# Optimization experiments

Hardware: AMD Instinct MI355X
Metric: run time of the kernel (lower is better)

The kernel has to match this reference:

```python
import jax, jax.numpy as jnp
import numpy as np

B, L, N, C = 4, 12, 1024, 3
D = 32          # num_hidden
ND = 32         # node_hidden
TE = 10         # time_emb_dim
ST = 96         # tsformer/st hidden feat
GH = 64         # estimation-gate hidden
KS = 2          # diffusion orders (k_s)
NUM_FEAT = 1
TID, DIW = 288, 7


def random_walk(adj):
    # adj: [B,N,N]; (D^-1)(A+I) row-normalized random-walk matrix
    n = adj.shape[-1]
    adj = adj + jnp.eye(n, dtype=adj.dtype)[None]
    d = adj.sum(axis=2)
    d_inv = jnp.where(d == 0, 0.0, 1.0 / d)
    return adj * d_inv[:, :, None]  # diag_embed(d_inv) @ adj == row scaling


def setup_inputs() -> dict:
    key = jax.random.key(0)
    ks = jax.random.split(key, 16)
    s = 0.05
    return {
        "history_data": jax.random.uniform(ks[0], (B, L, N, C), dtype=jnp.float32),
        "hidden_states_st": jax.random.normal(ks[1], (B, N, L, ST), dtype=jnp.float32),
        "sampled_adj": jax.random.uniform(ks[2], (B, N, N), dtype=jnp.float32),
        "W_emb": jax.random.normal(ks[3], (NUM_FEAT, D), dtype=jnp.float32) * s,
        "b_emb": jnp.zeros((D,), jnp.float32),
        "W_st": jax.random.normal(ks[4], (ST, D), dtype=jnp.float32) * s,
        "b_st": jnp.zeros((D,), jnp.float32),
        "TiD_emb": jax.random.normal(ks[5], (TID, TE), dtype=jnp.float32) * s,
        "DiW_emb": jax.random.normal(ks[6], (DIW, TE), dtype=jnp.float32) * s,
        "node_emb_u": jax.random.normal(ks[7], (N, ND), dtype=jnp.float32) * s,
        "node_emb_d": jax.random.normal(ks[8], (N, ND), dtype=jnp.float32) * s,
        "W_g1": jax.random.normal(ks[9], (2 * TE + 2 * ND, GH), dtype=jnp.float32) * s,
        "b_g1": jnp.zeros((GH,), jnp.float32),
        "W_g2": jax.random.normal(ks[10], (GH, 1), dtype=jnp.float32) * s,
        "b_g2": jnp.zeros((1,), jnp.float32),
        "W_dif": jax.random.normal(ks[11], ((1 + 3 * KS) * D, D), dtype=jnp.float32) * s,
        "b_dif": jnp.zeros((D,), jnp.float32),
    }


def reference(history_data, hidden_states_st, sampled_adj, W_emb, b_emb, W_st, b_st,
              TiD_emb, DiW_emb, node_emb_u, node_emb_d, W_g1, b_g1, W_g2, b_g2,
              W_dif, b_dif):
    # --- prepare inputs: time/node embedding gathers (D2STGNN._prepare_inputs) ---
    X = history_data.at[..., 2].multiply(1.0 / 7.0)
    t_idx = (X[..., NUM_FEAT] * TID).astype(jnp.int32)       # [B,L,N]
    d_idx = (X[..., NUM_FEAT + 1] * DIW).astype(jnp.int32)   # [B,L,N]
    T_D = TiD_emb[t_idx]   # [B,L,N,TE]
    D_W = DiW_emb[d_idx]   # [B,L,N,TE]
    Xf = X[..., :NUM_FEAT]  # [B,L,N,1]

    # --- graph construction (static self-adaptive + random-walk normalized learn graphs) ---
    static = jax.nn.softmax(jax.nn.relu(node_emb_d @ node_emb_u.T), axis=1)  # [N,N]
    rw_fwd = random_walk(sampled_adj)                       # [B,N,N]
    rw_bwd = random_walk(jnp.swapaxes(sampled_adj, -1, -2)) # [B,N,N]

    # --- input embedding + st hidden fusion ---
    H = jnp.einsum('blnf,fd->blnd', Xf, W_emb) + b_emb
    H_st = jnp.einsum('bnlk,kd->bnld', hidden_states_st, W_st) + b_st
    H = jax.nn.relu(H + jnp.transpose(H_st, (0, 2, 1, 3)))  # [B,L,N,D]

    # --- estimation (spatial) gate: sigmoid(FC(relu(FC([T_D,D_W,E_u,E_d])))) * X ---
    eu = jnp.broadcast_to(node_emb_u[None, None], (B, L, N, ND))
    ed = jnp.broadcast_to(node_emb_d[None, None], (B, L, N, ND))
    gate_feat = jnp.concatenate([T_D, D_W, eu, ed], axis=-1)  # [B,L,N,2TE+2ND]
    gate = jax.nn.sigmoid(jax.nn.relu(gate_feat @ W_g1 + b_g1) @ W_g2 + b_g2)  # [B,L,N,1]
    X_spa = H * gate

    # --- diffusion graph convolution over supports, KS orders each ---
    supports = [jnp.broadcast_to(static[None], (B, N, N)), rw_fwd, rw_bwd]
    outs = [X_spa]
    for A in supports:
        Z = X_spa
        for _ in range(KS):
            Z = jnp.einsum('bnm,blmd->blnd', A, Z)
            outs.append(Z)
    Hcat = jnp.concatenate(outs, axis=-1)  # [B,L,N,(1+3*KS)*D]
    out = Hcat @ W_dif + b_dif             # [B,L,N,D]
    return out
```

## Files before the change

kernel.cpp:

```cpp
#include <hip/hip_runtime.h>
#include <hip/hip_bf16.h>
#include <cstdint>

#define NN 1024
#define BBATCH 4
#define LLEN 12
#define NJ 384
#define TIDC 288
#define DIWC 7

typedef __attribute__((ext_vector_type(8))) short short8;
typedef __attribute__((ext_vector_type(4))) float f32x4;

__device__ inline ushort f2bf(float f) {
    unsigned u = __float_as_uint(f);
    u += 0x7FFFu + ((u >> 16) & 1u);
    return (ushort)(u >> 16);
}
__device__ inline float bf2f(ushort u) { return __uint_as_float(((unsigned)u) << 16); }

__global__ __launch_bounds__(256) void k_static(const float* __restrict__ emb_u,
                                                const float* __restrict__ emb_d,
                                                ushort* __restrict__ S_bf) {
    int i = blockIdx.x;
    int t = threadIdx.x;
    __shared__ float drow[32];
    __shared__ float red[256];
    if (t < 32) drow[t] = emb_d[i * 32 + t];
    __syncthreads();
    float v[4];
    float lsum = 0.f;
    for (int jj = 0; jj < 4; ++jj) {
        int j = jj * 256 + t;
        const float4* u4 = reinterpret_cast<const float4*>(emb_u + (size_t)j * 32);
        float acc = 0.f;
#pragma unroll
        for (int k4 = 0; k4 < 8; ++k4) {
            float4 u = u4[k4];
            acc += drow[k4 * 4 + 0] * u.x + drow[k4 * 4 + 1] * u.y +
                   drow[k4 * 4 + 2] * u.z + drow[k4 * 4 + 3] * u.w;
        }
        acc = fmaxf(acc, 0.f);
        v[jj] = __expf(acc);
        lsum += v[jj];
    }
    red[t] = lsum;
    __syncthreads();
    for (int s = 128; s > 0; s >>= 1) {
        if (t < s) red[t] += red[t + s];
        __syncthreads();
    }
    float inv = 1.f / red[0];
    for (int jj = 0; jj < 4; ++jj) S_bf[(size_t)i * NN + jj * 256 + t] = f2bf(v[jj] * inv);
}

__global__ __launch_bounds__(256) void k_adj_pre(const float* __restrict__ adj,
                                                 ushort* __restrict__ adjF,
                                                 ushort* __restrict__ adjT,
                                                 float* __restrict__ rs,
                                                 float* __restrict__ cs) {
    __shared__ float tile[64][65];
    int b = blockIdx.z;
    int r0 = blockIdx.y * 64, c0 = blockIdx.x * 64;
    int t = threadIdx.x;
    int col = (t & 15) * 4, rb = t >> 4;
#pragma unroll
    for (int i = 0; i < 4; ++i) {
        int r = rb + i * 16;
        float4 v = *reinterpret_cast<const float4*>(&adj[((size_t)b * NN + r0 + r) * NN + c0 + col]);
        tile[r][col] = v.x; tile[r][col + 1] = v.y; tile[r][col + 2] = v.z; tile[r][col + 3] = v.w;
        unsigned lo = (unsigned)f2bf(v.x) | ((unsigned)f2bf(v.y) << 16);
        unsigned hi = (unsigned)f2bf(v.z) | ((unsigned)f2bf(v.w) << 16);
        *reinterpret_cast<uint2*>(&adjF[((size_t)b * NN + r0 + r) * NN + c0 + col]) = make_uint2(lo, hi);
    }
    __syncthreads();
    {
        int r4 = t >> 2, q4 = t & 3;
        float s1 = 0.f;
#pragma unroll
        for (int c = 0; c < 16; ++c) s1 += tile[r4][q4 * 16 + c];
        s1 += __shfl_xor(s1, 1, 64);
        s1 += __shfl_xor(s1, 2, 64);
        if (q4 == 0) atomicAdd(&rs[b * NN + r0 + r4], s1);
        float s2 = 0.f;
#pragma unroll
        for (int rr = 0; rr < 16; ++rr) s2 += tile[q4 * 16 + rr][r4];
        s2 += __shfl_xor(s2, 1, 64);
        s2 += __shfl_xor(s2, 2, 64);
        if (q4 == 0) atomicAdd(&cs[b * NN + c0 + r4], s2);
    }
    int j = t >> 2, ch = t & 3;
    short8 o0, o1;
#pragma unroll
    for (int q = 0; q < 8; ++q) o0[q] = (short)f2bf(tile[ch * 16 + q][j]);
#pragma unroll
    for (int q = 0; q < 8; ++q) o1[q] = (short)f2bf(tile[ch * 16 + 8 + q][j]);
    size_t orow = ((size_t)b * NN + c0 + j) * NN + r0 + ch * 16;
    *(short8*)&adjT[orow] = o0;
    *(short8*)&adjT[orow + 8] = o1;
}

__global__ __launch_bounds__(64) void k_gate_pre(const float* __restrict__ emb_u,
                                                 const float* __restrict__ emb_d,
                                                 const float* __restrict__ W_g1,
                                                 const float* __restrict__ b_g1,
                                                 const float* __restrict__ TiD,
                                                 const float* __restrict__ DiW,
                                                 const float* __restrict__ W_st,
                                                 const float* __restrict__ W_dif,
                                                 float* __restrict__ U1, float* __restrict__ T1,
                                                 float* __restrict__ D1,
                                                 ushort* __restrict__ WstT_bf,
                                                 ushort* __restrict__ WdT_bf) {
    int r = blockIdx.x;
    int h = threadIdx.x;
    if (r < NN) {
        float acc = b_g1[h];
        for (int i = 0; i < 32; ++i) acc = fmaf(emb_u[r * 32 + i], W_g1[(20 + i) * 64 + h], acc);
        for (int i = 0; i < 32; ++i) acc = fmaf(emb_d[r * 32 + i], W_g1[(52 + i) * 64 + h], acc);
        U1[r * 64 + h] = acc;
    } else if (r < NN + TIDC) {
        int tt = r - NN;
        float acc = 0.f;
        for (int i = 0; i < 10; ++i) acc = fmaf(TiD[tt * 10 + i], W_g1[i * 64 + h], acc);
        T1[tt * 64 + h] = acc;
    } else if (r < NN + TIDC + DIWC) {
        int dd = r - (NN + TIDC);
        float acc = 0.f;
        for (int i = 0; i < 10; ++i) acc = fmaf(DiW[dd * 10 + i], W_g1[(10 + i) * 64 + h], acc);
        D1[dd * 64 + h] = acc;
    } else if (r == NN + TIDC + DIWC) {
        for (int i = h; i < 32 * 96; i += 64) WstT_bf[i] = f2bf(W_st[(i % 96) * 32 + i / 96]);
    } else {
        for (int i = h; i < 32 * 224; i += 64) WdT_bf[i] = f2bf(W_dif[(i % 224) * 32 + i / 224]);
    }
}

__global__ __launch_bounds__(256) void k_xspa(const float* __restrict__ hist,
                                              const float* __restrict__ hs,
                                              const float* __restrict__ W_emb,
                                              const float* __restrict__ b_emb,
                                              const float* __restrict__ b_st,
                                              const float* __restrict__ U1,
                                              const float* __restrict__ T1,
                                              const float* __restrict__ D1,
                                              const float* __restrict__ W_g2,
                                              const float* __restrict__ b_g2,
                                              const float* __restrict__ b_dif,
                                              const ushort* __restrict__ WstT_bf,
                                              const ushort* __restrict__ WdT_bf,
                                              ushort* __restrict__ XT,
                                              float* __restrict__ out) {
    __shared__ __align__(16) ushort hsm[64][104];
    __shared__ __align__(16) ushort Wst_s[32][104];
    __shared__ __align__(16) ushort Hs_bf[64][40];
    __shared__ __align__(16) ushort W0_s[32][40];
    __shared__ float gateL[64];
    __shared__ float histL[192];
    int t = threadIdx.x;
    int n0 = blockIdx.x * 64;
    int l = blockIdx.y;
    int b = blockIdx.z;
    for (int i = t; i < 384; i += 256) {
        int d = i / 12, c = i % 12;
        *(short8*)&Wst_s[d][c * 8] = *(const short8*)&WstT_bf[d * 96 + c * 8];
    }
    if (t < 128) {
        int d = t >> 2, c = t & 3;
        *(short8*)&W0_s[d][c * 8] = *(const short8*)&WdT_bf[d * 224 + c * 8];
    }
    if (t < 48)
        *(float4*)&histL[t * 4] =
            *(const float4*)&hist[(((size_t)b * LLEN + l) * NN + n0) * 3 + t * 4];
#pragma unroll
    for (int rr = 0; rr < 6; ++rr) {
        int i = t + 256 * rr;
        int s = i / 24, c = i % 24;
        float4 v = *(const float4*)&hs[(((size_t)b * NN + n0 + s) * LLEN + l) * 96 + c * 4];
        ushort4 u;
        u.x = f2bf(v.x); u.y = f2bf(v.y); u.z = f2bf(v.z); u.w = f2bf(v.w);
        *(ushort4*)&hsm[s][c * 4] = u;
    }
    __syncthreads();
    {
        int s = t >> 2, q = t & 3;
        int n = n0 + s;
        float x1 = histL[s * 3 + 1];
        float x2 = histL[s * 3 + 2] * (1.f / 7.f);
        int ti = (int)(x1 * 288.f); ti = ti < 0 ? 0 : (ti > 287 ? 287 : ti);
        int di = (int)(x2 * 7.f);   di = di < 0 ? 0 : (di > 6 ? 6 : di);
        const float* up = U1 + n * 64 + q * 16;
        const float* tp = T1 + ti * 64 + q * 16;
        const float* dp = D1 + di * 64 + q * 16;
        const float* wp = W_g2 + q * 16;
        float a = 0.f;
#pragma unroll
        for (int hh = 0; hh < 16; ++hh)
            a = fmaf(fmaxf(up[hh] + tp[hh] + dp[hh], 0.f), wp[hh], a);
        a += __shfl_xor(a, 1, 64);
        a += __shfl_xor(a, 2, 64);
        if (q == 0) gateL[s] = 1.f / (1.f + __expf(-(a + b_g2[0])));
    }
    int w = t >> 6, l6 = t & 63, lr = l6 & 15, lg = l6 >> 4;
    f32x4 hacc[2];
    hacc[0] = (f32x4){0.f, 0.f, 0.f, 0.f};
    hacc[1] = (f32x4){0.f, 0.f, 0.f, 0.f};
#pragma unroll
    for (int kc = 0; kc < 3; ++kc) {
        short8 a = *(const short8*)&hsm[w * 16 + lr][kc * 32 + lg * 8];
        short8 b0 = *(const short8*)&Wst_s[lr][kc * 32 + lg * 8];
        short8 b1 = *(const short8*)&Wst_s[16 + lr][kc * 32 + lg * 8];
        hacc[0] = __builtin_amdgcn_mfma_f32_16x16x32_bf16(a, b0, hacc[0], 0, 0, 0);
        hacc[1] = __builtin_amdgcn_mfma_f32_16x16x32_bf16(a, b1, hacc[1], 0, 0, 0);
    }
#pragma unroll
    for (int h = 0; h < 2; ++h) {
        int d = h * 16 + lr;
        float we = W_emb[d];
        float bb = b_emb[d] + b_st[d];
#pragma unroll
        for (int r = 0; r < 4; ++r) {
            int s = w * 16 + lg * 4 + r;
            float v = fmaxf(fmaf(histL[s * 3], we, bb) + hacc[h][r], 0.f);
            Hs_bf[s][d] = f2bf(v);
        }
    }
    __syncthreads();
    f32x4 oacc[2];
    oacc[0] = (f32x4){0.f, 0.f, 0.f, 0.f};
    oacc[1] = (f32x4){0.f, 0.f, 0.f, 0.f};
    {
        short8 a = *(const short8*)&Hs_bf[w * 16 + lr][lg * 8];
        short8 b0 = *(const short8*)&W0_s[lr][lg * 8];
        short8 b1 = *(const short8*)&W0_s[16 + lr][lg * 8];
        oacc[0] = __builtin_amdgcn_mfma_f32_16x16x32_bf16(a, b0, oacc[0], 0, 0, 0);
        oacc[1] = __builtin_amdgcn_mfma_f32_16x16x32_bf16(a, b1, oacc[1], 0, 0, 0);
    }
#pragma unroll
    for (int h = 0; h < 2; ++h) {
        int d = h * 16 + lr;
        float bd = b_dif[d];
#pragma unroll
        for (int r = 0; r < 4; ++r) {
            int s = w * 16 + lg * 4 + r;
            out[(((size_t)b * LLEN + l) * NN + n0 + s) * 32 + d] = fmaf(gateL[s], oacc[h][r], bd);
        }
    }
    {
        int dd = t >> 3, c = t & 7;
        short8 v;
#pragma unroll
        for (int i = 0; i < 8; ++i) {
            int s = c * 8 + i;
            v[i] = (short)f2bf(bf2f(Hs_bf[s][dd]) * gateL[s]);
        }
        *(short8*)&XT[((size_t)b * NJ + l * 32 + dd) * NN + n0 + c * 8] = v;
    }
}

#define DIFF_LOAD(ra, rw, kt)                                          \
    {                                                                  \
        const ushort* qA = pA + (size_t)(kt) * 64;                     \
        const ushort* qW = pW + (size_t)(kt) * 64;                     \
        _Pragma("unroll") for (int i = 0; i < 4; ++i)                  \
            ra[i] = *(const short8*)(qA + i * 8);                      \
        _Pragma("unroll") for (int i = 0; i < 2; ++i)                  \
            rw[i] = *(const short8*)(qW + i * 8);                      \
    }
#define DIFF_WRITE(buf, ra, rw)                                        \
    {                                                                  \
        _Pragma("unroll") for (int i = 0; i < 4; ++i)                  \
            *(short8*)&As[buf][arow * 64 + (((ac + i) ^ (arow & 7)) * 8)] = ra[i]; \
        _Pragma("unroll") for (int i = 0; i < 2; ++i)                  \
            *(short8*)&Ws[buf][wrow * 64 + (((wc + i) ^ (wrow & 7)) * 8)] = rw[i]; \
    }
#define DIFF_COMPUTE(buf)                                              \
    {                                                                  \
        _Pragma("unroll") for (int kk = 0; kk < 2; ++kk) {             \
            short8 af[4], bff[2];                                      \
            _Pragma("unroll") for (int mf = 0; mf < 4; ++mf) {         \
                int row = wm * 64 + mf * 16 + lr;                      \
                af[mf] = *(const short8*)&As[buf][row * 64 + (((kk * 4 + lg) ^ (row & 7)) * 8)]; \
            }                                                          \
            _Pragma("unroll") for (int nf = 0; nf < 2; ++nf) {         \
                int row = wn * 32 + nf * 16 + lr;                      \
                bff[nf] = *(const short8*)&Ws[buf][row * 64 + (((kk * 4 + lg) ^ (row & 7)) * 8)]; \
            }                                                          \
            _Pragma("unroll") for (int mf = 0; mf < 4; ++mf) {         \
                acc[mf][0] = __builtin_amdgcn_mfma_f32_16x16x32_bf16(af[mf], bff[0], acc[mf][0], 0, 0, 0); \
                acc[mf][1] = __builtin_amdgcn_mfma_f32_16x16x32_bf16(af[mf], bff[1], acc[mf][1], 0, 0, 0); \
            }                                                          \
        }                                                              \
    }

__global__ __launch_bounds__(256) void k_diff3(const ushort* __restrict__ S_bf,
                                               const ushort* __restrict__ adjF,
                                               const ushort* __restrict__ adjT,
                                               const float* __restrict__ rs,
                                               const float* __restrict__ cs,
                                               const ushort* __restrict__ In0,
                                               int in_per_chain,
                                               ushort* __restrict__ Out0) {
    __shared__ __align__(16) ushort As[2][128 * 64];
    __shared__ __align__(16) ushort Ws[2][64 * 64];
    int bid = blockIdx.x + 3 * blockIdx.y + 48 * blockIdx.z;
    int swz = (bid & 7) * 72 + (bid >> 3);
    int zz = swz / 48;
    int rem = swz % 48;
    int xx = rem >> 4, yy = rem & 15;
    int s = zz >> 2, b = zz & 3;
    int j0 = xx * 128;
    int n0 = yy * 64;
    const size_t ZT = (size_t)BBATCH * NJ * NN;
    const ushort* Wb = (s == 0) ? S_bf
                     : (s == 1) ? adjF + (size_t)b * NN * NN
                                : adjT + (size_t)b * NN * NN;
    const float* deg = (s == 0) ? nullptr : (s == 1 ? rs : cs);
    const ushort* Inb = In0 + (in_per_chain ? (size_t)s * ZT : 0) + (size_t)b * NJ * NN;
    ushort* Outb = Out0 + (size_t)s * ZT + (size_t)b * NJ * NN;

    int t = threadIdx.x;
    int arow = t >> 1, ac = (t & 1) * 4;
    int wrow = t >> 2, wc = (t & 3) * 2;
    const ushort* pA = Inb + (size_t)(j0 + arow) * NN + ac * 8;
    const ushort* pW = Wb + (size_t)(n0 + wrow) * NN + wc * 8;
    int w = t >> 6, wm = w >> 1, wn = w & 1;
    int l = t & 63, lr = l & 15, lg = l >> 4;
    f32x4 acc[4][2];
#pragma unroll
    for (int i = 0; i < 4; ++i)
#pragma unroll
        for (int j = 0; j < 2; ++j) acc[i][j] = (f32x4){0.f, 0.f, 0.f, 0.f};

    short8 raA[4], rwA[2], raB[4], rwB[2];
    DIFF_LOAD(raA, rwA, 0);
    DIFF_LOAD(raB, rwB, 1);
    DIFF_WRITE(0, raA, rwA);
    __syncthreads();
    int cur = 0;
#pragma unroll 1
    for (int kt2 = 0; kt2 < 16; kt2 += 2) {
        if (kt2 + 2 < 16) DIFF_LOAD(raA, rwA, kt2 + 2);
        DIFF_COMPUTE(cur);
        DIFF_WRITE(cur ^ 1, raB, rwB);
        __syncthreads();
        cur ^= 1;
        if (kt2 + 3 < 16) DIFF_LOAD(raB, rwB, kt2 + 3);
        DIFF_COMPUTE(cur);
        if (kt2 + 2 < 16) DIFF_WRITE(cur ^ 1, raA, rwA);
        __syncthreads();
        cur ^= 1;
    }
    bool resid = (deg != nullptr);
#pragma unroll
    for (int nf = 0; nf < 2; ++nf) {
        int n_g = n0 + wn * 32 + nf * 16 + lr;
        float scale = 1.f;
        if (resid) scale = 1.f / (deg[b * NN + n_g] + 1.f);
#pragma unroll
        for (int mf = 0; mf < 4; ++mf) {
#pragma unroll
            for (int r = 0; r < 4; ++r) {
                int j_g = j0 + wm * 64 + mf * 16 + lg * 4 + r;
                float v = acc[mf][nf][r];
                if (resid) v += bf2f(Inb[(size_t)j_g * NN + n_g]);
                v *= scale;
                Outb[(size_t)j_g * NN + n_g] = f2bf(v);
            }
        }
    }
}

__global__ __launch_bounds__(256) void k_zmfma(const ushort* __restrict__ Z1,
                                               const ushort* __restrict__ Z2,
                                               const ushort* __restrict__ WdT_bf,
                                               float* __restrict__ out) {
    __shared__ __align__(16) ushort zT[64][200];
    __shared__ __align__(16) ushort Wd_s[32][200];
    const size_t ZT = (size_t)BBATCH * NJ * NN;
    int t = threadIdx.x;
    int n0 = blockIdx.x * 64;
    int l = blockIdx.y;
    int b = blockIdx.z;
    for (int i = t; i < 768; i += 256) {
        int d = i / 24, c = i % 24;
        *(short8*)&Wd_s[d][c * 8] = *(const short8*)&WdT_bf[d * 224 + 32 + c * 8];
    }
    {
        int j = t >> 3, ch = t & 7;
#pragma unroll
        for (int c = 0; c < 6; ++c) {
            const ushort* Zp = ((c & 1) ? Z2 : Z1) + (size_t)(c >> 1) * ZT;
            short8 v = *(const short8*)&Zp[((size_t)b * NJ + l * 32 + j) * NN + n0 + ch * 8];
#pragma unroll
            for (int q = 0; q < 8; ++q) zT[ch * 8 + q][c * 32 + j] = (ushort)v[q];
        }
    }
    __syncthreads();
    int w = t >> 6, l6 = t & 63, lr = l6 & 15, lg = l6 >> 4;
    f32x4 acc[2];
    acc[0] = (f32x4){0.f, 0.f, 0.f, 0.f};
    acc[1] = (f32x4){0.f, 0.f, 0.f, 0.f};
#pragma unroll
    for (int kc = 0; kc < 6; ++kc) {
        short8 a = *(const short8*)&zT[w * 16 + lr][kc * 32 + lg * 8];
        short8 b0 = *(const short8*)&Wd_s[lr][kc * 32 + lg * 8];
        short8 b1 = *(const short8*)&Wd_s[16 + lr][kc * 32 + lg * 8];
        acc[0] = __builtin_amdgcn_mfma_f32_16x16x32_bf16(a, b0, acc[0], 0, 0, 0);
        acc[1] = __builtin_amdgcn_mfma_f32_16x16x32_bf16(a, b1, acc[1], 0, 0, 0);
    }
#pragma unroll
    for (int h = 0; h < 2; ++h) {
        int d = h * 16 + lr;
#pragma unroll
        for (int r = 0; r < 4; ++r) {
            int s = w * 16 + lg * 4 + r;
            size_t oi = (((size_t)b * LLEN + l) * NN + n0 + s) * 32 + d;
            out[oi] += acc[h][r];
        }
    }
}

extern "C" void kernel_launch(void* const* d_in, const int* in_sizes, int n_in,
                              void* d_out, int out_size, void* d_ws, size_t ws_size,
                              hipStream_t stream) {
    (void)in_sizes; (void)n_in; (void)out_size; (void)ws_size;
    const float* hist  = (const float*)d_in[0];
    const float* hs    = (const float*)d_in[1];
    const float* adj   = (const float*)d_in[2];
    const float* W_emb = (const float*)d_in[3];
    const float* b_emb = (const float*)d_in[4];
    const float* W_st  = (const float*)d_in[5];
    const float* b_st  = (const float*)d_in[6];
    const float* TiD   = (const float*)d_in[7];
    const float* DiW   = (const float*)d_in[8];
    const float* emb_u = (const float*)d_in[9];
    const float* emb_d = (const float*)d_in[10];
    const float* W_g1  = (const float*)d_in[11];
    const float* b_g1  = (const float*)d_in[12];
    const float* W_g2  = (const float*)d_in[13];
    const float* b_g2  = (const float*)d_in[14];
    const float* W_dif = (const float*)d_in[15];
    const float* b_dif = (const float*)d_in[16];
    float* out = (float*)d_out;

    uint8_t* w8 = (uint8_t*)d_ws;
    ushort* adjF = (ushort*)w8;
    ushort* adjT = (ushort*)(w8 + 8388608);
    ushort* S_bf = (ushort*)(w8 + 16777216);
    ushort* XT   = (ushort*)(w8 + 18874368);
    ushort* Z1   = (ushort*)(w8 + 22020096);
    ushort* Z2   = (ushort*)(w8 + 31457280);
    float*  rs   = (float*)(w8 + 40894464);
    float*  cs   = (float*)(w8 + 40910848);
    float*  U1   = (float*)(w8 + 40927232);
    float*  T1   = (float*)(w8 + 41189376);
    float*  D1   = (float*)(w8 + 41263104);
    ushort* WstT_bf = (ushort*)(w8 + 41264896);
    ushort* WdT_bf  = (ushort*)(w8 + 41271040);

    hipMemsetAsync(rs, 0, 2 * BBATCH * NN * sizeof(float), stream);
    k_adj_pre<<<dim3(16, 16, 4), 256, 0, stream>>>(adj, adjF, adjT, rs, cs);
    k_gate_pre<<<NN + TIDC + DIWC + 2, 64, 0, stream>>>(emb_u, emb_d, W_g1, b_g1, TiD, DiW,
                                                        W_st, W_dif, U1, T1, D1, WstT_bf, WdT_bf);
    k_static<<<NN, 256, 0, stream>>>(emb_u, emb_d, S_bf);
    k_xspa<<<dim3(16, 12, 4), 256, 0, stream>>>(hist, hs, W_emb, b_emb, b_st, U1, T1, D1,
                                                W_g2, b_g2, b_dif, WstT_bf, WdT_bf, XT, out);
    dim3 dgrid(3, 16, 12);
    k_diff3<<<dgrid, 256, 0, stream>>>(S_bf, adjF, adjT, rs, cs, XT, 0, Z1);
    k_diff3<<<dgrid, 256, 0, stream>>>(S_bf, adjF, adjT, rs, cs, Z1, 1, Z2);
    k_zmfma<<<dim3(16, 12, 4), 256, 0, stream>>>(Z1, Z2, WdT_bf, out);
}
```

Measured before the change: 211.5 us.

## Merge preprocessing kernels and stage diffusion tiles via direct global-to-LDS loads

Merges the three preprocessing kernels (adjacency transpose and degree sums, static softmax adjacency, gate precompute) into one launch that branches on block index. This cuts launch overhead and lets the independent pieces run at the same time. The diffusion GEMM replaces its register-staged double buffer with global_load_lds async copies straight into swizzled LDS. That removes the register round trip and simplifies the loop to one stage per k-tile. The risk is that the async LDS loads need correct waitcnt and barrier ordering, and the per-lane swizzle layout must match what the compute path reads.

```diff
diff --git a/kernel.cpp b/kernel.cpp
--- a/kernel.cpp
+++ b/kernel.cpp
@@ -12,6 +12,9 @@
 typedef __attribute__((ext_vector_type(8))) short short8;
 typedef __attribute__((ext_vector_type(4))) float f32x4;
 
+typedef __attribute__((address_space(1))) const void* gas_ptr;
+typedef __attribute__((address_space(3))) void* las_ptr;
+
 __device__ inline ushort f2bf(float f) {
     unsigned u = __float_as_uint(f);
     u += 0x7FFFu + ((u >> 16) & 1u);
@@ -19,120 +22,120 @@
 }
 __device__ inline float bf2f(ushort u) { return __uint_as_float(((unsigned)u) << 16); }
 
-__global__ __launch_bounds__(256) void k_static(const float* __restrict__ emb_u,
-                                                const float* __restrict__ emb_d,
-                                                ushort* __restrict__ S_bf) {
-    int i = blockIdx.x;
+__global__ __launch_bounds__(256) void k_pre(const float* __restrict__ adj,
+                                             ushort* __restrict__ adjF,
+                                             ushort* __restrict__ adjT,
+                                             float* __restrict__ rs,
+                                             float* __restrict__ cs,
+                                             const float* __restrict__ emb_u,
+                                             const float* __restrict__ emb_d,
+                                             ushort* __restrict__ S_bf,
+                                             const float* __restrict__ W_g1,
+                                             const float* __restrict__ b_g1,
+                                             const float* __restrict__ TiD,
+                                             const float* __restrict__ DiW,
+                                             const float* __restrict__ W_st,
+                                             const float* __restrict__ W_dif,
+                                             float* __restrict__ U1,
+                                             float* __restrict__ T1,
+                                             float* __restrict__ D1,
+                                             ushort* __restrict__ WstT_bf,
+                                             ushort* __restrict__ WdT_bf) {
+    __shared__ float smem[64 * 65];
+    int bid = blockIdx.x;
     int t = threadIdx.x;
-    __shared__ float drow[32];
-    __shared__ float red[256];
-    if (t < 32) drow[t] = emb_d[i * 32 + t];
-    __syncthreads();
-    float v[4];
-    float lsum = 0.f;
-    for (int jj = 0; jj < 4; ++jj) {
-        int j = jj * 256 + t;
-        const float4* u4 = reinterpret_cast<const float4*>(emb_u + (size_t)j * 32);
-        float acc = 0.f;
-#pragma unroll
-        for (int k4 = 0; k4 < 8; ++k4) {
-            float4 u = u4[k4];
-            acc += drow[k4 * 4 + 0] * u.x + drow[k4 * 4 + 1] * u.y +
-                   drow[k4 * 4 + 2] * u.z + drow[k4 * 4 + 3] * u.w;
-        }
-        acc = fmaxf(acc, 0.f);
-        v[jj] = __expf(acc);
-        lsum += v[jj];
-    }
-    red[t] = lsum;
-    __syncthreads();
-    for (int s = 128; s > 0; s >>= 1) {
-        if (t < s) red[t] += red[t + s];
+    if (bid < 1024) {
+        float (*tile)[65] = (float(*)[65])smem;
+        int b = bid >> 8;
+        int r0 = ((bid >> 4) & 15) * 64, c0 = (bid & 15) * 64;
+        int col = (t & 15) * 4, rb = t >> 4;
+#pragma unroll
+        for (int i = 0; i < 4; ++i) {
+            int r = rb + i * 16;
+            float4 v = *reinterpret_cast<const float4*>(&adj[((size_t)b * NN + r0 + r) * NN + c0 + col]);
+            tile[r][col] = v.x; tile[r][col + 1] = v.y; tile[r][col + 2] = v.z; tile[r][col + 3] = v.w;
+            unsigned lo = (unsigned)f2bf(v.x) | ((unsigned)f2bf(v.y) << 16);
+            unsigned hi = (unsigned)f2bf(v.z) | ((unsigned)f2bf(v.w) << 16);
+            *reinterpret_cast<uint2*>(&adjF[((size_t)b * NN + r0 + r) * NN + c0 + col]) = make_uint2(lo, hi);
+        }
         __syncthreads();
-    }
-    float inv = 1.f / red[0];
-    for (int jj = 0; jj < 4; ++jj) S_bf[(size_t)i * NN + jj * 256 + t] = f2bf(v[jj] * inv);
-}
-
-__global__ __launch_bounds__(256) void k_adj_pre(const float* __restrict__ adj,
-                                                 ushort* __restrict__ adjF,
-                                                 ushort* __restrict__ adjT,
-                                                 float* __restrict__ rs,
-                                                 float* __restrict__ cs) {
-    __shared__ float tile[64][65];
-    int b = blockIdx.z;
-    int r0 = blockIdx.y * 64, c0 = blockIdx.x * 64;
-    int t = threadIdx.x;
-    int col = (t & 15) * 4, rb = t >> 4;
-#pragma unroll
-    for (int i = 0; i < 4; ++i) {
-        int r = rb + i * 16;
-        float4 v = *reinterpret_cast<const float4*>(&adj[((size_t)b * NN + r0 + r) * NN + c0 + col]);
-        tile[r][col] = v.x; tile[r][col + 1] = v.y; tile[r][col + 2] = v.z; tile[r][col + 3] = v.w;
-        unsigned lo = (unsigned)f2bf(v.x) | ((unsigned)f2bf(v.y) << 16);
-        unsigned hi = (unsigned)f2bf(v.z) | ((unsigned)f2bf(v.w) << 16);
-        *reinterpret_cast<uint2*>(&adjF[((size_t)b * NN + r0 + r) * NN + c0 + col]) = make_uint2(lo, hi);
-    }
-    __syncthreads();
-    {
-        int r4 = t >> 2, q4 = t & 3;
-        float s1 = 0.f;
-#pragma unroll
-        for (int c = 0; c < 16; ++c) s1 += tile[r4][q4 * 16 + c];
-        s1 += __shfl_xor(s1, 1, 64);
-        s1 += __shfl_xor(s1, 2, 64);
-        if (q4 == 0) atomicAdd(&rs[b * NN + r0 + r4], s1);
-        float s2 = 0.f;
-#pragma unroll
-        for (int rr = 0; rr < 16; ++rr) s2 += tile[q4 * 16 + rr][r4];
-        s2 += __shfl_xor(s2, 1, 64);
-        s2 += __shfl_xor(s2, 2, 64);
-        if (q4 == 0) atomicAdd(&cs[b * NN + c0 + r4], s2);
-    }
-    int j = t >> 2, ch = t & 3;
-    short8 o0, o1;
-#pragma unroll
-    for (int q = 0; q < 8; ++q) o0[q] = (short)f2bf(tile[ch * 16 + q][j]);
-#pragma unroll
-    for (int q = 0; q < 8; ++q) o1[q] = (short)f2bf(tile[ch * 16 + 8 + q][j]);
-    size_t orow = ((size_t)b * NN + c0 + j) * NN + r0 + ch * 16;
-    *(short8*)&adjT[orow] = o0;
-    *(short8*)&adjT[orow + 8] = o1;
-}
-
-__global__ __launch_bounds__(64) void k_gate_pre(const float* __restrict__ emb_u,
-                                                 const float* __restrict__ emb_d,
-                                                 const float* __restrict__ W_g1,
-                                                 const float* __restrict__ b_g1,
-                                                 const float* __restrict__ TiD,
-                                                 const float* __restrict__ DiW,
-                                                 const float* __restrict__ W_st,
-                                                 const float* __restrict__ W_dif,
-                                                 float* __restrict__ U1, float* __restrict__ T1,
-                                                 float* __restrict__ D1,
-                                                 ushort* __restrict__ WstT_bf,
-                                                 ushort* __restrict__ WdT_bf) {
-    int r = blockIdx.x;
-    int h = threadIdx.x;
-    if (r < NN) {
-        float acc = b_g1[h];
-        for (int i = 0; i < 32; ++i) acc = fmaf(emb_u[r * 32 + i], W_g1[(20 + i) * 64 + h], acc);
-        for (int i = 0; i < 32; ++i) acc = fmaf(emb_d[r * 32 + i], W_g1[(52 + i) * 64 + h], acc);
-        U1[r * 64 + h] = acc;
-    } else if (r < NN + TIDC) {
-        int tt = r - NN;
-        float acc = 0.f;
-        for (int i = 0; i < 10; ++i) acc = fmaf(TiD[tt * 10 + i], W_g1[i * 64 + h], acc);
-        T1[tt * 64 + h] = acc;
-    } else if (r < NN + TIDC + DIWC) {
-        int dd = r - (NN + TIDC);
-        float acc = 0.f;
-        for (int i = 0; i < 10; ++i) acc = fmaf(DiW[dd * 10 + i], W_g1[(10 + i) * 64 + h], acc);
-        D1[dd * 64 + h] = acc;
-    } else if (r == NN + TIDC + DIWC) {
-        for (int i = h; i < 32 * 96; i += 64) WstT_bf[i] = f2bf(W_st[(i % 96) * 32 + i / 96]);
+        {
+            int r4 = t >> 2, q4 = t & 3;
+            float s1 = 0.f;
+#pragma unroll
+            for (int c = 0; c < 16; ++c) s1 += tile[r4][q4 * 16 + c];
+            s1 += __shfl_xor(s1, 1, 64);
+            s1 += __shfl_xor(s1, 2, 64);
+            if (q4 == 0) atomicAdd(&rs[b * NN + r0 + r4], s1);
+            float s2 = 0.f;
+#pragma unroll
+            for (int rr = 0; rr < 16; ++rr) s2 += tile[q4 * 16 + rr][r4];
+            s2 += __shfl_xor(s2, 1, 64);
+            s2 += __shfl_xor(s2, 2, 64);
+            if (q4 == 0) atomicAdd(&cs[b * NN + c0 + r4], s2);
+        }
+        int j = t >> 2, ch = t & 3;
+        short8 o0, o1;
+#pragma unroll
+        for (int q = 0; q < 8; ++q) o0[q] = (short)f2bf(tile[ch * 16 + q][j]);
+#pragma unroll
+        for (int q = 0; q < 8; ++q) o1[q] = (short)f2bf(tile[ch * 16 + 8 + q][j]);
+        size_t orow = ((size_t)b * NN + c0 + j) * NN + r0 + ch * 16;
+        *(short8*)&adjT[orow] = o0;
+        *(short8*)&adjT[orow + 8] = o1;
+    } else if (bid < 2048) {
+        int i = bid - 1024;
+        float* drow = smem;
+        float* red = smem + 32;
+        if (t < 32) drow[t] = emb_d[i * 32 + t];
+        __syncthreads();
+        float v[4];
+        float lsum = 0.f;
+        for (int jj = 0; jj < 4; ++jj) {
+            int j = jj * 256 + t;
+            const float4* u4 = reinterpret_cast<const float4*>(emb_u + (size_t)j * 32);
+            float acc = 0.f;
+#pragma unroll
+            for (int k4 = 0; k4 < 8; ++k4) {
+                float4 u = u4[k4];
+                acc += drow[k4 * 4 + 0] * u.x + drow[k4 * 4 + 1] * u.y +
+                       drow[k4 * 4 + 2] * u.z + drow[k4 * 4 + 3] * u.w;
+            }
+            acc = fmaxf(acc, 0.f);
+            v[jj] = __expf(acc);
+            lsum += v[jj];
+        }
+        red[t] = lsum;
+        __syncthreads();
+        for (int s = 128; s > 0; s >>= 1) {
+            if (t < s) red[t] += red[t + s];
+            __syncthreads();
+        }
+        float inv = 1.f / red[0];
+        for (int jj = 0; jj < 4; ++jj) S_bf[(size_t)i * NN + jj * 256 + t] = f2bf(v[jj] * inv);
     } else {
-        for (int i = h; i < 32 * 224; i += 64) WdT_bf[i] = f2bf(W_dif[(i % 224) * 32 + i / 224]);
+        int r = (bid - 2048) * 4 + (t >> 6);
+        int h = t & 63;
+        if (r < NN) {
+            float acc = b_g1[h];
+            for (int i = 0; i < 32; ++i) acc = fmaf(emb_u[r * 32 + i], W_g1[(20 + i) * 64 + h], acc);
+            for (int i = 0; i < 32; ++i) acc = fmaf(emb_d[r * 32 + i], W_g1[(52 + i) * 64 + h], acc);
+            U1[r * 64 + h] = acc;
+        } else if (r < NN + TIDC) {
+            int tt = r - NN;
+            float acc = 0.f;
+            for (int i = 0; i < 10; ++i) acc = fmaf(TiD[tt * 10 + i], W_g1[i * 64 + h], acc);
+            T1[tt * 64 + h] = acc;
+        } else if (r < NN + TIDC + DIWC) {
+            int dd = r - (NN + TIDC);
+            float acc = 0.f;
+            for (int i = 0; i < 10; ++i) acc = fmaf(DiW[dd * 10 + i], W_g1[(10 + i) * 64 + h], acc);
+            D1[dd * 64 + h] = acc;
+        } else if (r == NN + TIDC + DIWC) {
+            for (int i = h; i < 32 * 96; i += 64) WstT_bf[i] = f2bf(W_st[(i % 96) * 32 + i / 96]);
+        } else if (r == NN + TIDC + DIWC + 1) {
+            for (int i = h; i < 32 * 224; i += 64) WdT_bf[i] = f2bf(W_dif[(i % 224) * 32 + i / 224]);
+        }
     }
 }
 
@@ -258,21 +261,18 @@
     }
 }
 
-#define DIFF_LOAD(ra, rw, kt)                                          \
-    {                                                                  \
-        const ushort* qA = pA + (size_t)(kt) * 64;                     \
-        const ushort* qW = pW + (size_t)(kt) * 64;                     \
-        _Pragma("unroll") for (int i = 0; i < 4; ++i)                  \
-            ra[i] = *(const short8*)(qA + i * 8);                      \
-        _Pragma("unroll") for (int i = 0; i < 2; ++i)                  \
-            rw[i] = *(const short8*)(qW + i * 8);                      \
-    }
-#define DIFF_WRITE(buf, ra, rw)                                        \
-    {                                                                  \
-        _Pragma("unroll") for (int i = 0; i < 4; ++i)                  \
-            *(short8*)&As[buf][arow * 64 + (((ac + i) ^ (arow & 7)) * 8)] = ra[i]; \
-        _Pragma("unroll") for (int i = 0; i < 2; ++i)                  \
-            *(short8*)&Ws[buf][wrow * 64 + (((wc + i) ^ (wrow & 7)) * 8)] = rw[i]; \
+#define STAGE(buf, kt)                                                              \
+    {                                                                               \
+        const ushort* gA = pA + (size_t)(kt) * 64;                                  \
+        const ushort* gW = pW + (size_t)(kt) * 64;                                  \
+        _Pragma("unroll") for (int i = 0; i < 4; ++i)                               \
+            __builtin_amdgcn_global_load_lds(                                        \
+                (gas_ptr)(gA + aoff[i]),                                             \
+                (las_ptr)&As[buf][(w * 32 + i * 8) * 64], 16, 0, 0);                \
+        _Pragma("unroll") for (int i = 0; i < 2; ++i)                               \
+            __builtin_amdgcn_global_load_lds(                                        \
+                (gas_ptr)(gW + woff[i]),                                             \
+                (las_ptr)&Ws[buf][(w * 16 + i * 8) * 64], 16, 0, 0);                \
     }
 #define DIFF_COMPUTE(buf)                                              \
     {                                                                  \
@@ -320,34 +320,35 @@
     ushort* Outb = Out0 + (size_t)s * ZT + (size_t)b * NJ * NN;
 
     int t = threadIdx.x;
-    int arow = t >> 1, ac = (t & 1) * 4;
-    int wrow = t >> 2, wc = (t & 3) * 2;
-    const ushort* pA = Inb + (size_t)(j0 + arow) * NN + ac * 8;
-    const ushort* pW = Wb + (size_t)(n0 + wrow) * NN + wc * 8;
     int w = t >> 6, wm = w >> 1, wn = w & 1;
     int l = t & 63, lr = l & 15, lg = l >> 4;
+    int rl = l >> 3, c8 = l & 7;
+    size_t aoff[4], woff[2];
+#pragma unroll
+    for (int i = 0; i < 4; ++i) {
+        int row = w * 32 + i * 8 + rl;
+        aoff[i] = (size_t)row * NN + (size_t)((c8 ^ (row & 7)) * 8);
+    }
+#pragma unroll
+    for (int i = 0; i < 2; ++i) {
+        int row = w * 16 + i * 8 + rl;
+        woff[i] = (size_t)row * NN + (size_t)((c8 ^ (row & 7)) * 8);
+    }
+    const ushort* pA = Inb + (size_t)j0 * NN;
+    const ushort* pW = Wb + (size_t)n0 * NN;
     f32x4 acc[4][2];
 #pragma unroll
     for (int i = 0; i < 4; ++i)
 #pragma unroll
         for (int j = 0; j < 2; ++j) acc[i][j] = (f32x4){0.f, 0.f, 0.f, 0.f};
 
-    short8 raA[4], rwA[2], raB[4], rwB[2];
-    DIFF_LOAD(raA, rwA, 0);
-    DIFF_LOAD(raB, rwB, 1);
-    DIFF_WRITE(0, raA, rwA);
+    STAGE(0, 0);
     __syncthreads();
     int cur = 0;
 #pragma unroll 1
-    for (int kt2 = 0; kt2 < 16; kt2 += 2) {
-        if (kt2 + 2 < 16) DIFF_LOAD(raA, rwA, kt2 + 2);
+    for (int kt = 0; kt < 16; ++kt) {
+        if (kt < 15) STAGE(cur ^ 1, kt + 1);
         DIFF_COMPUTE(cur);
-        DIFF_WRITE(cur ^ 1, raB, rwB);
-        __syncthreads();
-        cur ^= 1;
-        if (kt2 + 3 < 16) DIFF_LOAD(raB, rwB, kt2 + 3);
-        DIFF_COMPUTE(cur);
-        if (kt2 + 2 < 16) DIFF_WRITE(cur ^ 1, raA, rwA);
         __syncthreads();
         cur ^= 1;
     }
@@ -460,10 +461,9 @@
     ushort* WdT_bf  = (ushort*)(w8 + 41271040);
 
     hipMemsetAsync(rs, 0, 2 * BBATCH * NN * sizeof(float), stream);
-    k_adj_pre<<<dim3(16, 16, 4), 256, 0, stream>>>(adj, adjF, adjT, rs, cs);
-    k_gate_pre<<<NN + TIDC + DIWC + 2, 64, 0, stream>>>(emb_u, emb_d, W_g1, b_g1, TiD, DiW,
-                                                        W_st, W_dif, U1, T1, D1, WstT_bf, WdT_bf);
-    k_static<<<NN, 256, 0, stream>>>(emb_u, emb_d, S_bf);
+    k_pre<<<2379, 256, 0, stream>>>(adj, adjF, adjT, rs, cs, emb_u, emb_d, S_bf,
+                                    W_g1, b_g1, TiD, DiW, W_st, W_dif,
+                                    U1, T1, D1, WstT_bf, WdT_bf);
     k_xspa<<<dim3(16, 12, 4), 256, 0, stream>>>(hist, hs, W_emb, b_emb, b_st, U1, T1, D1,
                                                 W_g2, b_g2, b_dif, WstT_bf, WdT_bf, XT, out);
     dim3 dgrid(3, 16, 12);
```

New measurement: 196.0 us. 1.08x faster.
